# Performance work log

Hardware: AMD Instinct MI355X
Metric: run time of the kernel (lower is better)

The kernel has to match this reference:

```python
import jax, jax.numpy as jnp
import numpy as np

N = 50000      # num nodes
HID = 64       # hidden_dim
N2V = 64       # node2vec dim
E = 800000     # num edges
EP = 100000    # prediction edges
L = 2          # num_layers
EPS = 1e-5     # BatchNorm eps


def setup_inputs() -> dict:
    key = jax.random.key(0)
    ks = jax.random.split(key, 8)
    edge_index = jax.random.randint(ks[0], (2, E), 0, N)
    pred_edge = jax.random.randint(ks[1], (EP, 2), 0, N)
    id_emb = jax.random.normal(ks[2], (N, HID), jnp.float32) * 0.1      # learnable ID embedding
    n2v_emb = jax.random.normal(ks[3], (N, N2V), jnp.float32) * 0.1     # frozen node2vec embedding
    proj_w = jax.random.normal(ks[4], (HID + N2V, HID), jnp.float32) / np.sqrt(HID + N2V)
    proj_b = jnp.zeros((HID,), jnp.float32)
    conv_w = jax.random.normal(ks[5], (L, HID, HID), jnp.float32) / np.sqrt(HID)
    conv_b = jnp.zeros((L, HID), jnp.float32)
    bn_gamma = jnp.ones((L, HID), jnp.float32)
    bn_beta = jnp.zeros((L, HID), jnp.float32)
    return {"edge_index": edge_index, "pred_edge": pred_edge, "id_emb": id_emb,
            "n2v_emb": n2v_emb, "proj_w": proj_w, "proj_b": proj_b,
            "conv_w": conv_w, "conv_b": conv_b, "bn_gamma": bn_gamma, "bn_beta": bn_beta}


def reference(edge_index, pred_edge, id_emb, n2v_emb, proj_w, proj_b, conv_w, conv_b, bn_gamma, bn_beta):
    # input projection of concatenated embeddings: [N, HID+N2V] @ [HID+N2V, HID]
    x = jnp.concatenate([id_emb, n2v_emb], axis=1) @ proj_w + proj_b

    # GCN normalization with self-loops: norm_e = d^-1/2[src] * d^-1/2[dst]
    loops = jnp.arange(N, dtype=edge_index.dtype)
    row = jnp.concatenate([edge_index[0], loops])   # source nodes
    col = jnp.concatenate([edge_index[1], loops])   # destination nodes
    deg = jax.ops.segment_sum(jnp.ones(row.shape, x.dtype), col, num_segments=N)
    dis = jnp.where(deg > 0, jax.lax.rsqrt(deg), 0.0)
    norm = dis[row] * dis[col]                      # [E+N]

    for l in range(L):
        h = x @ conv_w[l]                                                    # [N, HID]
        agg = jax.ops.segment_sum(norm[:, None] * h[row], col, num_segments=N) + conv_b[l]
        # BatchNorm1d (training-mode batch stats over nodes)
        mu = agg.mean(axis=0)
        var = agg.var(axis=0)
        xn = (agg - mu) * jax.lax.rsqrt(var + EPS) * bn_gamma[l] + bn_beta[l]
        x = x + jax.nn.relu(xn)                                              # residual (shapes match)

    # dot-product link decoder
    z = x
    return (z[pred_edge[:, 0]] * z[pred_edge[:, 1]]).sum(axis=1)
```

## Files before the change

kernel.cpp:

```cpp
#include <hip/hip_runtime.h>

#define NN 50000
#define HID 64
#define NE 800000
#define NP 100000
#define BN_EPS 1e-5f
#define NB1 196

static inline size_t alignup(size_t x) { return (x + 255) & ~(size_t)255; }

__device__ __forceinline__ void f4fma(float a, const float4& w, float4& c) {
    c.x += a * w.x; c.y += a * w.y; c.z += a * w.z; c.w += a * w.w;
}
__device__ __forceinline__ void f4acc(float w, const float4& a, float4& c) {
    c.x += w * a.x; c.y += w * a.y; c.z += w * a.z; c.w += w * a.w;
}
__device__ __forceinline__ unsigned bfpack(float a, float b) {
    unsigned ua = __float_as_uint(a), ub = __float_as_uint(b);
    ua = (ua + 0x7fffu + ((ua >> 16) & 1u)) >> 16;
    ub = (ub + 0x7fffu + ((ub >> 16) & 1u)) >> 16;
    return ua | (ub << 16);
}
__device__ __forceinline__ float4 bf2f4(uint2 u) {
    float4 r;
    r.x = __uint_as_float(u.x << 16);
    r.y = __uint_as_float(u.x & 0xffff0000u);
    r.z = __uint_as_float(u.y << 16);
    r.w = __uint_as_float(u.y & 0xffff0000u);
    return r;
}


__global__ __launch_bounds__(256) void k_zero(int* __restrict__ cnt, float* __restrict__ sums) {
    int i = blockIdx.x * blockDim.x + threadIdx.x;
    if (i < NN) cnt[i] = 0;
    if (i < 256) sums[i] = 0.f;
}


__global__ __launch_bounds__(256) void k_count(const int* __restrict__ col,
                                               int* __restrict__ cnt, int* __restrict__ rank) {
    int e = blockIdx.x * blockDim.x + threadIdx.x;
    if (e < NE) rank[e] = atomicAdd(&cnt[col[e]], 1);
}

__global__ __launch_bounds__(256) void k_dis(const int* __restrict__ cnt, float* __restrict__ dis) {
    int i = blockIdx.x * blockDim.x + threadIdx.x;
    if (i < NN) dis[i] = rsqrtf((float)(cnt[i] + 1));
}


__global__ __launch_bounds__(256) void k_scan1(const int* __restrict__ cnt,
                                               int* __restrict__ offs, int* __restrict__ bsum) {
    __shared__ int s[256];
    int t = threadIdx.x;
    int i = blockIdx.x * 256 + t;
    int v = (i < NN) ? cnt[i] : 0;
    s[t] = v;
    __syncthreads();
    for (int off = 1; off < 256; off <<= 1) {
        int add = (t >= off) ? s[t - off] : 0;
        __syncthreads();
        s[t] += add;
        __syncthreads();
    }
    if (i < NN) offs[i] = s[t] - v;
    if (t == 255) bsum[blockIdx.x] = s[255];
}

__global__ __launch_bounds__(256) void k_scan2(int* __restrict__ bsum, int* __restrict__ boff) {
    __shared__ int s[256];
    int t = threadIdx.x;
    int v = (t < NB1) ? bsum[t] : 0;
    s[t] = v;
    __syncthreads();
    for (int off = 1; off < 256; off <<= 1) {
        int add = (t >= off) ? s[t - off] : 0;
        __syncthreads();
        s[t] += add;
        __syncthreads();
    }
    if (t < NB1) boff[t] = s[t] - v;
}

__global__ __launch_bounds__(256) void k_scan3(int* __restrict__ offs, const int* __restrict__ boff) {
    int i = blockIdx.x * blockDim.x + threadIdx.x;
    if (i < NN) offs[i] += boff[i >> 8];
    if (i == 0) offs[NN] = NE;
}


__global__ __launch_bounds__(256) void k_fill(const int* __restrict__ row, const int* __restrict__ col,
                                              const int* __restrict__ rank, const int* __restrict__ offs,
                                              const float* __restrict__ dis,
                                              int2* __restrict__ csr) {
    int e = blockIdx.x * blockDim.x + threadIdx.x;
    if (e >= NE) return;
    int s = row[e], d = col[e];
    int2 v;
    v.x = s;
    v.y = __float_as_int(dis[s] * dis[d]);
    csr[offs[d] + rank[e]] = v;
}


__global__ __launch_bounds__(256) void k_proj(const float* __restrict__ id_emb,
                                              const float* __restrict__ n2v,
                                              const float* __restrict__ W,
                                              const float* __restrict__ b,
                                              float* __restrict__ x,
                                              unsigned short* __restrict__ xh) {
    __shared__ float A[64 * 132];
    __shared__ float Wl[128 * 64];
    int tid = threadIdx.x;
    int node0 = blockIdx.x * 64;
    for (int i = tid; i < 128 * 64; i += 256) Wl[i] = W[i];
    for (int i = tid; i < 64 * 128; i += 256) {
        int r = i >> 7, k = i & 127;
        int n = node0 + r;
        float v = 0.f;
        if (n < NN) v = (k < 64) ? id_emb[n * 64 + k] : n2v[n * 64 + (k - 64)];
        A[r * 132 + k] = v;
    }
    __syncthreads();
    int sub = tid >> 4, q = tid & 15;
    const float4* W4 = (const float4*)Wl;
    float4 bb = ((const float4*)b)[q];
    float4 c0 = bb, c1 = bb, c2 = bb, c3 = bb;
#pragma unroll 4
    for (int k4 = 0; k4 < 32; ++k4) {
        int k = k4 * 4;
        float4 w0 = W4[(k + 0) * 16 + q];
        float4 w1 = W4[(k + 1) * 16 + q];
        float4 w2 = W4[(k + 2) * 16 + q];
        float4 w3 = W4[(k + 3) * 16 + q];
        float4 a;
        a = *(const float4*)&A[(sub * 4 + 0) * 132 + k];
        f4fma(a.x, w0, c0); f4fma(a.y, w1, c0); f4fma(a.z, w2, c0); f4fma(a.w, w3, c0);
        a = *(const float4*)&A[(sub * 4 + 1) * 132 + k];
        f4fma(a.x, w0, c1); f4fma(a.y, w1, c1); f4fma(a.z, w2, c1); f4fma(a.w, w3, c1);
        a = *(const float4*)&A[(sub * 4 + 2) * 132 + k];
        f4fma(a.x, w0, c2); f4fma(a.y, w1, c2); f4fma(a.z, w2, c2); f4fma(a.w, w3, c2);
        a = *(const float4*)&A[(sub * 4 + 3) * 132 + k];
        f4fma(a.x, w0, c3); f4fma(a.y, w1, c3); f4fma(a.z, w2, c3); f4fma(a.w, w3, c3);
    }
    float4* x4 = (float4*)x;
    uint2* xh2 = (uint2*)xh;
    int n0 = node0 + sub * 4;
    if (n0 + 0 < NN) { x4[(n0+0)*16+q] = c0; xh2[(n0+0)*16+q] = make_uint2(bfpack(c0.x,c0.y), bfpack(c0.z,c0.w)); }
    if (n0 + 1 < NN) { x4[(n0+1)*16+q] = c1; xh2[(n0+1)*16+q] = make_uint2(bfpack(c1.x,c1.y), bfpack(c1.z,c1.w)); }
    if (n0 + 2 < NN) { x4[(n0+2)*16+q] = c2; xh2[(n0+2)*16+q] = make_uint2(bfpack(c2.x,c2.y), bfpack(c2.z,c2.w)); }
    if (n0 + 3 < NN) { x4[(n0+3)*16+q] = c3; xh2[(n0+3)*16+q] = make_uint2(bfpack(c3.x,c3.y), bfpack(c3.z,c3.w)); }
}


__global__ __launch_bounds__(256) void k_gather(const int* __restrict__ offs,
                                                const int2* __restrict__ csr,
                                                const float* __restrict__ dis,
                                                const float* __restrict__ x,
                                                const unsigned short* __restrict__ xh,
                                                float* __restrict__ t) {
    int gw = (blockIdx.x * blockDim.x + threadIdx.x) >> 6;
    int lane = threadIdx.x & 63;
    int sub = lane >> 4, q = lane & 15;
    int node = gw * 4 + sub;
    if (node >= NN) return;
    const float4* x4 = (const float4*)x;
    const uint2* xh2 = (const uint2*)xh;
    float di = dis[node];
    float dd = di * di;
    float4 v = x4[node * 16 + q];
    float4 acc = make_float4(dd * v.x, dd * v.y, dd * v.z, dd * v.w);
    int j = offs[node], j1 = offs[node + 1];
    for (; j + 3 < j1; j += 4) {
        int2 e0 = csr[j], e1 = csr[j + 1], e2 = csr[j + 2], e3 = csr[j + 3];
        uint2 u0 = xh2[e0.x * 16 + q];
        uint2 u1 = xh2[e1.x * 16 + q];
        uint2 u2 = xh2[e2.x * 16 + q];
        uint2 u3 = xh2[e3.x * 16 + q];
        f4acc(__int_as_float(e0.y), bf2f4(u0), acc);
        f4acc(__int_as_float(e1.y), bf2f4(u1), acc);
        f4acc(__int_as_float(e2.y), bf2f4(u2), acc);
        f4acc(__int_as_float(e3.y), bf2f4(u3), acc);
    }
    for (; j < j1; ++j) {
        int2 e0 = csr[j];
        uint2 u0 = xh2[e0.x * 16 + q];
        f4acc(__int_as_float(e0.y), bf2f4(u0), acc);
    }
    ((float4*)t)[node * 16 + q] = acc;
}


__global__ __launch_bounds__(256) void k_gemm_stats(const float* __restrict__ t,
                                                    const float* __restrict__ W,
                                                    float* __restrict__ agg,
                                                    float* __restrict__ sums) {
    __shared__ float T[64 * 68];
    __shared__ float Wl[64 * 64];
    __shared__ float ls0[16][64];
    __shared__ float ls1[16][64];
    int tid = threadIdx.x;
    for (int i = tid; i < 64 * 64; i += 256) Wl[i] = W[i];
    int sub = tid >> 4, q = tid & 15;
    const float4* t4 = (const float4*)t;
    const float4* W4 = (const float4*)Wl;
    float4* agg4 = (float4*)agg;
    float4 s1 = make_float4(0.f, 0.f, 0.f, 0.f), s2 = s1;
    const int ngroups = (NN + 63) / 64;
    for (int g = blockIdx.x; g < ngroups; g += gridDim.x) {
        __syncthreads();
        for (int i = tid; i < 1024; i += 256) {
            int r = i >> 4, c4 = i & 15;
            int n = g * 64 + r;
            float4 v = (n < NN) ? t4[n * 16 + c4] : make_float4(0.f, 0.f, 0.f, 0.f);
            *((float4*)(T + r * 68 + c4 * 4)) = v;
        }
        __syncthreads();
        float4 c0 = make_float4(0.f,0.f,0.f,0.f), c1 = c0, c2 = c0, c3 = c0;
#pragma unroll 8
        for (int k = 0; k < 64; ++k) {
            float4 w = W4[k * 16 + q];
            float a0 = T[(sub * 4 + 0) * 68 + k];
            float a1 = T[(sub * 4 + 1) * 68 + k];
            float a2 = T[(sub * 4 + 2) * 68 + k];
            float a3 = T[(sub * 4 + 3) * 68 + k];
            f4fma(a0, w, c0);
            f4fma(a1, w, c1);
            f4fma(a2, w, c2);
            f4fma(a3, w, c3);
        }
        int nrow = g * 64 + sub * 4;
        if (nrow + 0 < NN) { agg4[(nrow + 0) * 16 + q] = c0;
            s1.x += c0.x; s1.y += c0.y; s1.z += c0.z; s1.w += c0.w;
            s2.x += c0.x*c0.x; s2.y += c0.y*c0.y; s2.z += c0.z*c0.z; s2.w += c0.w*c0.w; }
        if (nrow + 1 < NN) { agg4[(nrow + 1) * 16 + q] = c1;
            s1.x += c1.x; s1.y += c1.y; s1.z += c1.z; s1.w += c1.w;
            s2.x += c1.x*c1.x; s2.y += c1.y*c1.y; s2.z += c1.z*c1.z; s2.w += c1.w*c1.w; }
        if (nrow + 2 < NN) { agg4[(nrow + 2) * 16 + q] = c2;
            s1.x += c2.x; s1.y += c2.y; s1.z += c2.z; s1.w += c2.w;
            s2.x += c2.x*c2.x; s2.y += c2.y*c2.y; s2.z += c2.z*c2.z; s2.w += c2.w*c2.w; }
        if (nrow + 3 < NN) { agg4[(nrow + 3) * 16 + q] = c3;
            s1.x += c3.x; s1.y += c3.y; s1.z += c3.z; s1.w += c3.w;
            s2.x += c3.x*c3.x; s2.y += c3.y*c3.y; s2.z += c3.z*c3.z; s2.w += c3.w*c3.w; }
    }
    ls0[sub][q * 4 + 0] = s1.x; ls0[sub][q * 4 + 1] = s1.y;
    ls0[sub][q * 4 + 2] = s1.z; ls0[sub][q * 4 + 3] = s1.w;
    ls1[sub][q * 4 + 0] = s2.x; ls1[sub][q * 4 + 1] = s2.y;
    ls1[sub][q * 4 + 2] = s2.z; ls1[sub][q * 4 + 3] = s2.w;
    __syncthreads();
    if (tid < 64) {
        float a = 0.f;
#pragma unroll
        for (int r = 0; r < 16; ++r) a += ls0[r][tid];
        atomicAdd(&sums[tid], a);
    } else if (tid < 128) {
        int c = tid - 64;
        float a = 0.f;
#pragma unroll
        for (int r = 0; r < 16; ++r) a += ls1[r][c];
        atomicAdd(&sums[64 + c], a);
    }
}


__global__ __launch_bounds__(256) void k_bnupdate(const float* __restrict__ agg,
                                                  const float* __restrict__ sums,
                                                  const float* __restrict__ gamma,
                                                  const float* __restrict__ beta,
                                                  float* __restrict__ x,
                                                  unsigned short* __restrict__ xh) {
    int i = blockIdx.x * blockDim.x + threadIdx.x;
    if (i >= NN * 16) return;
    int f4 = i & 15;
    const float invn = 1.0f / (float)NN;
    float4 sm = ((const float4*)sums)[f4];
    float4 sq = ((const float4*)(sums + 64))[f4];
    float4 g = ((const float4*)gamma)[f4];
    float4 be = ((const float4*)beta)[f4];
    float4 a = ((const float4*)agg)[i];
    float4 xv = ((const float4*)x)[i];
    float mu, var, rstd, xn;
    mu = sm.x * invn; var = sq.x * invn - mu * mu; rstd = rsqrtf(var + BN_EPS);
    xn = (a.x - mu) * rstd * g.x + be.x; xv.x += fmaxf(xn, 0.f);
    mu = sm.y * invn; var = sq.y * invn - mu * mu; rstd = rsqrtf(var + BN_EPS);
    xn = (a.y - mu) * rstd * g.y + be.y; xv.y += fmaxf(xn, 0.f);
    mu = sm.z * invn; var = sq.z * invn - mu * mu; rstd = rsqrtf(var + BN_EPS);
    xn = (a.z - mu) * rstd * g.z + be.z; xv.z += fmaxf(xn, 0.f);
    mu = sm.w * invn; var = sq.w * invn - mu * mu; rstd = rsqrtf(var + BN_EPS);
    xn = (a.w - mu) * rstd * g.w + be.w; xv.w += fmaxf(xn, 0.f);
    ((float4*)x)[i] = xv;
    ((uint2*)xh)[i] = make_uint2(bfpack(xv.x, xv.y), bfpack(xv.z, xv.w));
}


__global__ __launch_bounds__(256) void k_decode(const int* __restrict__ pred,
                                                const unsigned short* __restrict__ zh,
                                                float* __restrict__ out) {
    int gw = (blockIdx.x * blockDim.x + threadIdx.x) >> 6;
    int lane = threadIdx.x & 63;
    int sub = lane >> 4, q = lane & 15;
    int p = gw * 4 + sub;
    if (p >= NP) return;
    const uint2* z2 = (const uint2*)zh;
    int a = pred[2 * p], b = pred[2 * p + 1];
    float4 va = bf2f4(z2[a * 16 + q]);
    float4 vb = bf2f4(z2[b * 16 + q]);
    float v = va.x * vb.x + va.y * vb.y + va.z * vb.z + va.w * vb.w;
    v += __shfl_xor(v, 1);
    v += __shfl_xor(v, 2);
    v += __shfl_xor(v, 4);
    v += __shfl_xor(v, 8);
    if (q == 0) out[p] = v;
}

extern "C" void kernel_launch(void* const* d_in, const int* in_sizes, int n_in,
                              void* d_out, int out_size, void* d_ws, size_t ws_size,
                              hipStream_t stream) {
    const int* edge_index = (const int*)d_in[0];
    const int* pred       = (const int*)d_in[1];
    const float* id_emb   = (const float*)d_in[2];
    const float* n2v      = (const float*)d_in[3];
    const float* proj_w   = (const float*)d_in[4];
    const float* proj_b   = (const float*)d_in[5];
    const float* conv_w   = (const float*)d_in[6];
    const float* gamma    = (const float*)d_in[8];
    const float* beta     = (const float*)d_in[9];
    float* out = (float*)d_out;

    char* ws = (char*)d_ws;
    size_t off = 0;
    float* dis  = (float*)(ws + off); off += alignup(NN * 4);
    int* cnt    = (int*)(ws + off);   off += alignup(NN * 4);
    int* offs   = (int*)(ws + off);   off += alignup((NN + 1) * 4);
    int* rank   = (int*)(ws + off);   off += alignup((size_t)NE * 4);
    int* bsum   = (int*)(ws + off);   off += alignup(NB1 * 4);
    int* boff   = (int*)(ws + off);   off += alignup(NB1 * 4);
    int2* csr   = (int2*)(ws + off);  off += alignup((size_t)NE * 8);
    float* x    = (float*)(ws + off); off += alignup((size_t)NN * 64 * 4);
    float* t    = (float*)(ws + off); off += alignup((size_t)NN * 64 * 4);
    float* agg  = (float*)(ws + off); off += alignup((size_t)NN * 64 * 4);
    unsigned short* xh = (unsigned short*)(ws + off); off += alignup((size_t)NN * 64 * 2);
    float* sums = (float*)(ws + off);

    const int* row = edge_index;
    const int* col = edge_index + NE;

    k_zero<<<NB1, 256, 0, stream>>>(cnt, sums);
    k_count<<<(NE + 255) / 256, 256, 0, stream>>>(col, cnt, rank);
    k_dis<<<(NN + 255) / 256, 256, 0, stream>>>(cnt, dis);
    k_scan1<<<NB1, 256, 0, stream>>>(cnt, offs, bsum);
    k_scan2<<<1, 256, 0, stream>>>(bsum, boff);
    k_scan3<<<NB1, 256, 0, stream>>>(offs, boff);
    k_fill<<<(NE + 255) / 256, 256, 0, stream>>>(row, col, rank, offs, dis, csr);

    k_proj<<<(NN + 63) / 64, 256, 0, stream>>>(id_emb, n2v, proj_w, proj_b, x, xh);

    for (int l = 0; l < 2; ++l) {
        k_gather<<<((NN + 3) / 4 * 64 + 255) / 256, 256, 0, stream>>>(offs, csr, dis, x, xh, t);
        k_gemm_stats<<<512, 256, 0, stream>>>(t, conv_w + l * 64 * 64, agg, sums + l * 128);
        k_bnupdate<<<(NN * 16 + 255) / 256, 256, 0, stream>>>(agg, sums + l * 128, gamma + l * 64, beta + l * 64, x, xh);
    }

    k_decode<<<(NP / 4 * 64 + 255) / 256, 256, 0, stream>>>(pred, xh, out);
}
```

Before: 221.5 us.

## Store gathered features in bf16, drop LDS staging in GEMMs, fuse dis into scan

The gather kernel now writes its aggregated features as packed bf16 instead of fp32, halving that intermediate's traffic, and the conv GEMM reads bf16 rows directly from global memory rather than staging tiles in shared memory. The input projection drops its shared-memory A tile, reads rows from global memory, and becomes a grid-stride kernel with 512 blocks. The degree-rsqrt kernel is folded into the first scan pass, and the gather loop unrolls 8 edges at a time. The extra bf16 rounding of the aggregate adds precision loss, and direct global reads repeated across the 16 column lanes rely on cache hits.

```diff
diff --git a/kernel.cpp b/kernel.cpp
--- a/kernel.cpp
+++ b/kernel.cpp
@@ -44,18 +44,15 @@
     if (e < NE) rank[e] = atomicAdd(&cnt[col[e]], 1);
 }
 
-__global__ __launch_bounds__(256) void k_dis(const int* __restrict__ cnt, float* __restrict__ dis) {
-    int i = blockIdx.x * blockDim.x + threadIdx.x;
-    if (i < NN) dis[i] = rsqrtf((float)(cnt[i] + 1));
-}
-
 
 __global__ __launch_bounds__(256) void k_scan1(const int* __restrict__ cnt,
-                                               int* __restrict__ offs, int* __restrict__ bsum) {
+                                               int* __restrict__ offs, int* __restrict__ bsum,
+                                               float* __restrict__ dis) {
     __shared__ int s[256];
     int t = threadIdx.x;
     int i = blockIdx.x * 256 + t;
     int v = (i < NN) ? cnt[i] : 0;
+    if (i < NN) dis[i] = rsqrtf((float)(v + 1));
     s[t] = v;
     __syncthreads();
     for (int off = 1; off < 256; off <<= 1) {
@@ -110,47 +107,58 @@
                                               const float* __restrict__ b,
                                               float* __restrict__ x,
                                               unsigned short* __restrict__ xh) {
-    __shared__ float A[64 * 132];
     __shared__ float Wl[128 * 64];
     int tid = threadIdx.x;
-    int node0 = blockIdx.x * 64;
     for (int i = tid; i < 128 * 64; i += 256) Wl[i] = W[i];
-    for (int i = tid; i < 64 * 128; i += 256) {
-        int r = i >> 7, k = i & 127;
-        int n = node0 + r;
-        float v = 0.f;
-        if (n < NN) v = (k < 64) ? id_emb[n * 64 + k] : n2v[n * 64 + (k - 64)];
-        A[r * 132 + k] = v;
-    }
     __syncthreads();
     int sub = tid >> 4, q = tid & 15;
     const float4* W4 = (const float4*)Wl;
-    float4 bb = ((const float4*)b)[q];
-    float4 c0 = bb, c1 = bb, c2 = bb, c3 = bb;
-#pragma unroll 4
-    for (int k4 = 0; k4 < 32; ++k4) {
-        int k = k4 * 4;
-        float4 w0 = W4[(k + 0) * 16 + q];
-        float4 w1 = W4[(k + 1) * 16 + q];
-        float4 w2 = W4[(k + 2) * 16 + q];
-        float4 w3 = W4[(k + 3) * 16 + q];
-        float4 a;
-        a = *(const float4*)&A[(sub * 4 + 0) * 132 + k];
-        f4fma(a.x, w0, c0); f4fma(a.y, w1, c0); f4fma(a.z, w2, c0); f4fma(a.w, w3, c0);
-        a = *(const float4*)&A[(sub * 4 + 1) * 132 + k];
-        f4fma(a.x, w0, c1); f4fma(a.y, w1, c1); f4fma(a.z, w2, c1); f4fma(a.w, w3, c1);
-        a = *(const float4*)&A[(sub * 4 + 2) * 132 + k];
-        f4fma(a.x, w0, c2); f4fma(a.y, w1, c2); f4fma(a.z, w2, c2); f4fma(a.w, w3, c2);
-        a = *(const float4*)&A[(sub * 4 + 3) * 132 + k];
-        f4fma(a.x, w0, c3); f4fma(a.y, w1, c3); f4fma(a.z, w2, c3); f4fma(a.w, w3, c3);
-    }
+    const float4* id4 = (const float4*)id_emb;
+    const float4* nv4 = (const float4*)n2v;
     float4* x4 = (float4*)x;
     uint2* xh2 = (uint2*)xh;
-    int n0 = node0 + sub * 4;
-    if (n0 + 0 < NN) { x4[(n0+0)*16+q] = c0; xh2[(n0+0)*16+q] = make_uint2(bfpack(c0.x,c0.y), bfpack(c0.z,c0.w)); }
-    if (n0 + 1 < NN) { x4[(n0+1)*16+q] = c1; xh2[(n0+1)*16+q] = make_uint2(bfpack(c1.x,c1.y), bfpack(c1.z,c1.w)); }
-    if (n0 + 2 < NN) { x4[(n0+2)*16+q] = c2; xh2[(n0+2)*16+q] = make_uint2(bfpack(c2.x,c2.y), bfpack(c2.z,c2.w)); }
-    if (n0 + 3 < NN) { x4[(n0+3)*16+q] = c3; xh2[(n0+3)*16+q] = make_uint2(bfpack(c3.x,c3.y), bfpack(c3.z,c3.w)); }
+    float4 bb = ((const float4*)b)[q];
+    const int ngroups = (NN + 63) / 64;
+    for (int g = blockIdx.x; g < ngroups; g += gridDim.x) {
+        int n0 = g * 64 + sub * 4;
+        int r0 = min(n0 + 0, NN - 1), r1 = min(n0 + 1, NN - 1);
+        int r2 = min(n0 + 2, NN - 1), r3 = min(n0 + 3, NN - 1);
+        float4 c0 = bb, c1 = bb, c2 = bb, c3 = bb;
+#pragma unroll 4
+        for (int k4 = 0; k4 < 16; ++k4) {
+            float4 a0 = id4[r0 * 16 + k4];
+            float4 a1 = id4[r1 * 16 + k4];
+            float4 a2 = id4[r2 * 16 + k4];
+            float4 a3 = id4[r3 * 16 + k4];
+            float4 w0 = W4[(k4 * 4 + 0) * 16 + q];
+            float4 w1 = W4[(k4 * 4 + 1) * 16 + q];
+            float4 w2 = W4[(k4 * 4 + 2) * 16 + q];
+            float4 w3 = W4[(k4 * 4 + 3) * 16 + q];
+            f4fma(a0.x, w0, c0); f4fma(a0.y, w1, c0); f4fma(a0.z, w2, c0); f4fma(a0.w, w3, c0);
+            f4fma(a1.x, w0, c1); f4fma(a1.y, w1, c1); f4fma(a1.z, w2, c1); f4fma(a1.w, w3, c1);
+            f4fma(a2.x, w0, c2); f4fma(a2.y, w1, c2); f4fma(a2.z, w2, c2); f4fma(a2.w, w3, c2);
+            f4fma(a3.x, w0, c3); f4fma(a3.y, w1, c3); f4fma(a3.z, w2, c3); f4fma(a3.w, w3, c3);
+        }
+#pragma unroll 4
+        for (int k4 = 0; k4 < 16; ++k4) {
+            float4 a0 = nv4[r0 * 16 + k4];
+            float4 a1 = nv4[r1 * 16 + k4];
+            float4 a2 = nv4[r2 * 16 + k4];
+            float4 a3 = nv4[r3 * 16 + k4];
+            float4 w0 = W4[(k4 * 4 + 64) * 16 + q];
+            float4 w1 = W4[(k4 * 4 + 65) * 16 + q];
+            float4 w2 = W4[(k4 * 4 + 66) * 16 + q];
+            float4 w3 = W4[(k4 * 4 + 67) * 16 + q];
+            f4fma(a0.x, w0, c0); f4fma(a0.y, w1, c0); f4fma(a0.z, w2, c0); f4fma(a0.w, w3, c0);
+            f4fma(a1.x, w0, c1); f4fma(a1.y, w1, c1); f4fma(a1.z, w2, c1); f4fma(a1.w, w3, c1);
+            f4fma(a2.x, w0, c2); f4fma(a2.y, w1, c2); f4fma(a2.z, w2, c2); f4fma(a2.w, w3, c2);
+            f4fma(a3.x, w0, c3); f4fma(a3.y, w1, c3); f4fma(a3.z, w2, c3); f4fma(a3.w, w3, c3);
+        }
+        if (n0 + 0 < NN) { x4[(n0+0)*16+q] = c0; xh2[(n0+0)*16+q] = make_uint2(bfpack(c0.x,c0.y), bfpack(c0.z,c0.w)); }
+        if (n0 + 1 < NN) { x4[(n0+1)*16+q] = c1; xh2[(n0+1)*16+q] = make_uint2(bfpack(c1.x,c1.y), bfpack(c1.z,c1.w)); }
+        if (n0 + 2 < NN) { x4[(n0+2)*16+q] = c2; xh2[(n0+2)*16+q] = make_uint2(bfpack(c2.x,c2.y), bfpack(c2.z,c2.w)); }
+        if (n0 + 3 < NN) { x4[(n0+3)*16+q] = c3; xh2[(n0+3)*16+q] = make_uint2(bfpack(c3.x,c3.y), bfpack(c3.z,c3.w)); }
+    }
 }
 
 
@@ -159,7 +167,7 @@
                                                 const float* __restrict__ dis,
                                                 const float* __restrict__ x,
                                                 const unsigned short* __restrict__ xh,
-                                                float* __restrict__ t) {
+                                                unsigned short* __restrict__ th) {
     int gw = (blockIdx.x * blockDim.x + threadIdx.x) >> 6;
     int lane = threadIdx.x & 63;
     int sub = lane >> 4, q = lane & 15;
@@ -172,75 +180,81 @@
     float4 v = x4[node * 16 + q];
     float4 acc = make_float4(dd * v.x, dd * v.y, dd * v.z, dd * v.w);
     int j = offs[node], j1 = offs[node + 1];
-    for (; j + 3 < j1; j += 4) {
-        int2 e0 = csr[j], e1 = csr[j + 1], e2 = csr[j + 2], e3 = csr[j + 3];
+    for (; j + 7 < j1; j += 8) {
+        int2 e0 = csr[j],     e1 = csr[j + 1], e2 = csr[j + 2], e3 = csr[j + 3];
+        int2 e4 = csr[j + 4], e5 = csr[j + 5], e6 = csr[j + 6], e7 = csr[j + 7];
         uint2 u0 = xh2[e0.x * 16 + q];
         uint2 u1 = xh2[e1.x * 16 + q];
         uint2 u2 = xh2[e2.x * 16 + q];
         uint2 u3 = xh2[e3.x * 16 + q];
+        uint2 u4 = xh2[e4.x * 16 + q];
+        uint2 u5 = xh2[e5.x * 16 + q];
+        uint2 u6 = xh2[e6.x * 16 + q];
+        uint2 u7 = xh2[e7.x * 16 + q];
         f4acc(__int_as_float(e0.y), bf2f4(u0), acc);
         f4acc(__int_as_float(e1.y), bf2f4(u1), acc);
         f4acc(__int_as_float(e2.y), bf2f4(u2), acc);
         f4acc(__int_as_float(e3.y), bf2f4(u3), acc);
+        f4acc(__int_as_float(e4.y), bf2f4(u4), acc);
+        f4acc(__int_as_float(e5.y), bf2f4(u5), acc);
+        f4acc(__int_as_float(e6.y), bf2f4(u6), acc);
+        f4acc(__int_as_float(e7.y), bf2f4(u7), acc);
     }
     for (; j < j1; ++j) {
         int2 e0 = csr[j];
         uint2 u0 = xh2[e0.x * 16 + q];
         f4acc(__int_as_float(e0.y), bf2f4(u0), acc);
     }
-    ((float4*)t)[node * 16 + q] = acc;
-}
-
-
-__global__ __launch_bounds__(256) void k_gemm_stats(const float* __restrict__ t,
+    ((uint2*)th)[node * 16 + q] = make_uint2(bfpack(acc.x, acc.y), bfpack(acc.z, acc.w));
+}
+
+
+__global__ __launch_bounds__(256) void k_gemm_stats(const unsigned short* __restrict__ th,
                                                     const float* __restrict__ W,
                                                     float* __restrict__ agg,
                                                     float* __restrict__ sums) {
-    __shared__ float T[64 * 68];
     __shared__ float Wl[64 * 64];
     __shared__ float ls0[16][64];
     __shared__ float ls1[16][64];
     int tid = threadIdx.x;
     for (int i = tid; i < 64 * 64; i += 256) Wl[i] = W[i];
+    __syncthreads();
     int sub = tid >> 4, q = tid & 15;
-    const float4* t4 = (const float4*)t;
+    const uint2* t2 = (const uint2*)th;
     const float4* W4 = (const float4*)Wl;
     float4* agg4 = (float4*)agg;
     float4 s1 = make_float4(0.f, 0.f, 0.f, 0.f), s2 = s1;
     const int ngroups = (NN + 63) / 64;
     for (int g = blockIdx.x; g < ngroups; g += gridDim.x) {
-        __syncthreads();
-        for (int i = tid; i < 1024; i += 256) {
-            int r = i >> 4, c4 = i & 15;
-            int n = g * 64 + r;
-            float4 v = (n < NN) ? t4[n * 16 + c4] : make_float4(0.f, 0.f, 0.f, 0.f);
-            *((float4*)(T + r * 68 + c4 * 4)) = v;
+        int n0 = g * 64 + sub * 4;
+        int r0 = min(n0 + 0, NN - 1), r1 = min(n0 + 1, NN - 1);
+        int r2 = min(n0 + 2, NN - 1), r3 = min(n0 + 3, NN - 1);
+        float4 c0 = make_float4(0.f,0.f,0.f,0.f), c1 = c0, c2 = c0, c3 = c0;
+#pragma unroll 4
+        for (int k4 = 0; k4 < 16; ++k4) {
+            float4 a0 = bf2f4(t2[r0 * 16 + k4]);
+            float4 a1 = bf2f4(t2[r1 * 16 + k4]);
+            float4 a2 = bf2f4(t2[r2 * 16 + k4]);
+            float4 a3 = bf2f4(t2[r3 * 16 + k4]);
+            float4 w0 = W4[(k4 * 4 + 0) * 16 + q];
+            float4 w1 = W4[(k4 * 4 + 1) * 16 + q];
+            float4 w2 = W4[(k4 * 4 + 2) * 16 + q];
+            float4 w3 = W4[(k4 * 4 + 3) * 16 + q];
+            f4fma(a0.x, w0, c0); f4fma(a0.y, w1, c0); f4fma(a0.z, w2, c0); f4fma(a0.w, w3, c0);
+            f4fma(a1.x, w0, c1); f4fma(a1.y, w1, c1); f4fma(a1.z, w2, c1); f4fma(a1.w, w3, c1);
+            f4fma(a2.x, w0, c2); f4fma(a2.y, w1, c2); f4fma(a2.z, w2, c2); f4fma(a2.w, w3, c2);
+            f4fma(a3.x, w0, c3); f4fma(a3.y, w1, c3); f4fma(a3.z, w2, c3); f4fma(a3.w, w3, c3);
         }
-        __syncthreads();
-        float4 c0 = make_float4(0.f,0.f,0.f,0.f), c1 = c0, c2 = c0, c3 = c0;
-#pragma unroll 8
-        for (int k = 0; k < 64; ++k) {
-            float4 w = W4[k * 16 + q];
-            float a0 = T[(sub * 4 + 0) * 68 + k];
-            float a1 = T[(sub * 4 + 1) * 68 + k];
-            float a2 = T[(sub * 4 + 2) * 68 + k];
-            float a3 = T[(sub * 4 + 3) * 68 + k];
-            f4fma(a0, w, c0);
-            f4fma(a1, w, c1);
-            f4fma(a2, w, c2);
-            f4fma(a3, w, c3);
-        }
-        int nrow = g * 64 + sub * 4;
-        if (nrow + 0 < NN) { agg4[(nrow + 0) * 16 + q] = c0;
+        if (n0 + 0 < NN) { agg4[(n0 + 0) * 16 + q] = c0;
             s1.x += c0.x; s1.y += c0.y; s1.z += c0.z; s1.w += c0.w;
             s2.x += c0.x*c0.x; s2.y += c0.y*c0.y; s2.z += c0.z*c0.z; s2.w += c0.w*c0.w; }
-        if (nrow + 1 < NN) { agg4[(nrow + 1) * 16 + q] = c1;
+        if (n0 + 1 < NN) { agg4[(n0 + 1) * 16 + q] = c1;
             s1.x += c1.x; s1.y += c1.y; s1.z += c1.z; s1.w += c1.w;
             s2.x += c1.x*c1.x; s2.y += c1.y*c1.y; s2.z += c1.z*c1.z; s2.w += c1.w*c1.w; }
-        if (nrow + 2 < NN) { agg4[(nrow + 2) * 16 + q] = c2;
+        if (n0 + 2 < NN) { agg4[(n0 + 2) * 16 + q] = c2;
             s1.x += c2.x; s1.y += c2.y; s1.z += c2.z; s1.w += c2.w;
             s2.x += c2.x*c2.x; s2.y += c2.y*c2.y; s2.z += c2.z*c2.z; s2.w += c2.w*c2.w; }
-        if (nrow + 3 < NN) { agg4[(nrow + 3) * 16 + q] = c3;
+        if (n0 + 3 < NN) { agg4[(n0 + 3) * 16 + q] = c3;
             s1.x += c3.x; s1.y += c3.y; s1.z += c3.z; s1.w += c3.w;
             s2.x += c3.x*c3.x; s2.y += c3.y*c3.y; s2.z += c3.z*c3.z; s2.w += c3.w*c3.w; }
     }
@@ -338,9 +352,9 @@
     int* boff   = (int*)(ws + off);   off += alignup(NB1 * 4);
     int2* csr   = (int2*)(ws + off);  off += alignup((size_t)NE * 8);
     float* x    = (float*)(ws + off); off += alignup((size_t)NN * 64 * 4);
-    float* t    = (float*)(ws + off); off += alignup((size_t)NN * 64 * 4);
     float* agg  = (float*)(ws + off); off += alignup((size_t)NN * 64 * 4);
     unsigned short* xh = (unsigned short*)(ws + off); off += alignup((size_t)NN * 64 * 2);
+    unsigned short* th = (unsigned short*)(ws + off); off += alignup((size_t)NN * 64 * 2);
     float* sums = (float*)(ws + off);
 
     const int* row = edge_index;
@@ -348,17 +362,16 @@
 
     k_zero<<<NB1, 256, 0, stream>>>(cnt, sums);
     k_count<<<(NE + 255) / 256, 256, 0, stream>>>(col, cnt, rank);
-    k_dis<<<(NN + 255) / 256, 256, 0, stream>>>(cnt, dis);
-    k_scan1<<<NB1, 256, 0, stream>>>(cnt, offs, bsum);
+    k_scan1<<<NB1, 256, 0, stream>>>(cnt, offs, bsum, dis);
     k_scan2<<<1, 256, 0, stream>>>(bsum, boff);
     k_scan3<<<NB1, 256, 0, stream>>>(offs, boff);
     k_fill<<<(NE + 255) / 256, 256, 0, stream>>>(row, col, rank, offs, dis, csr);
 
-    k_proj<<<(NN + 63) / 64, 256, 0, stream>>>(id_emb, n2v, proj_w, proj_b, x, xh);
+    k_proj<<<512, 256, 0, stream>>>(id_emb, n2v, proj_w, proj_b, x, xh);
 
     for (int l = 0; l < 2; ++l) {
-        k_gather<<<((NN + 3) / 4 * 64 + 255) / 256, 256, 0, stream>>>(offs, csr, dis, x, xh, t);
-        k_gemm_stats<<<512, 256, 0, stream>>>(t, conv_w + l * 64 * 64, agg, sums + l * 128);
+        k_gather<<<((NN + 3) / 4 * 64 + 255) / 256, 256, 0, stream>>>(offs, csr, dis, x, xh, th);
+        k_gemm_stats<<<512, 256, 0, stream>>>(th, conv_w + l * 64 * 64, agg, sums + l * 128);
         k_bnupdate<<<(NN * 16 + 255) / 256, 256, 0, stream>>>(agg, sums + l * 128, gamma + l * 64, beta + l * 64, x, xh);
     }
 
```

Result: faster. 213.0 us (-3.8%).
